# Performance work log

Hardware: AMD Instinct MI355X
Metric: run time of the kernel (lower is better)

The kernel has to match this reference:

```python
import jax, jax.numpy as jnp
import numpy as np

B, N = 16384, 2048
L = 1.0  # regularizer scale `l`


def setup_inputs() -> dict:
    key = jax.random.key(0)
    w = jax.random.normal(key, (B, N), dtype=jnp.float32)
    return {"w": w}


def reference(w):
    # Standardize each unit (column) over the batch; K.std is population std.
    mean = jnp.mean(w, axis=0)
    std = jnp.std(w, axis=0)
    fs = (w - mean) / std  # [B, N]

    # Original: for all P = N*(N-1)/2 pairs (i<j), loss_xy[b] = |mean_pairs(fs[b,i]*fs[b,j])|
    # (note K.mean axis=0 on the gathered [P, B] arrays reduces over PAIRS, per batch element).
    # Use the exact identity sum_{i<j} x_i x_j = ((sum x)^2 - sum x^2) / 2
    # to avoid materializing the O(N^2) gathered pairs.
    n = w.shape[1]
    s = jnp.sum(fs, axis=1)        # [B]
    s2 = jnp.sum(fs * fs, axis=1)  # [B]
    pair_mean = (s * s - s2) / (n * (n - 1))  # == sum_pairs / P, shape [B]

    return L * jnp.mean(jnp.abs(pair_mean))
```

## Files before the change

### kernel.cpp

```cpp
#include <hip/hip_runtime.h>
#include <math.h>

#define B_ROWS 16384
#define N_COLS 2048

#define WS_P2       0
#define WS_MEAN     (8 * 4096)
#define WS_INVSTD   (8 * 4096 + N_COLS)
#define WS_PARTIALS (8 * 4096 + 2 * N_COLS)

constexpr int K1_BLOCK = 256;
constexpr int K1_COLGROUPS = N_COLS / (K1_BLOCK * 4);
constexpr int K1_ROWCHUNKS = 1024;
constexpr int K1_ROWS_PER_CHUNK = B_ROWS / K1_ROWCHUNKS;

__global__ __launch_bounds__(K1_BLOCK) void colstats_kernel(
    const float* __restrict__ w, float* __restrict__ ws) {
  const int cg = blockIdx.x % K1_COLGROUPS;
  const int rc = blockIdx.x / K1_COLGROUPS;
  const int col4 = cg * K1_BLOCK + threadIdx.x;
  const int col = col4 * 4;
  const float4* __restrict__ w4 = reinterpret_cast<const float4*>(w);
  const int row_start = rc * K1_ROWS_PER_CHUNK;

  float sx = 0.f, sy = 0.f, sz = 0.f, sw = 0.f;
  float qx = 0.f, qy = 0.f, qz = 0.f, qw = 0.f;
#pragma unroll
  for (int r = 0; r < K1_ROWS_PER_CHUNK; ++r) {
    float4 v = w4[(size_t)(row_start + r) * (N_COLS / 4) + col4];
    sx += v.x; sy += v.y; sz += v.z; sw += v.w;
    qx = fmaf(v.x, v.x, qx);
    qy = fmaf(v.y, v.y, qy);
    qz = fmaf(v.z, v.z, qz);
    qw = fmaf(v.w, v.w, qw);
  }
  const int rg = rc >> 7;
  float* __restrict__ p2 = ws + WS_P2 + rg * 4096;
  atomicAdd(&p2[col + 0], sx);
  atomicAdd(&p2[col + 1], sy);
  atomicAdd(&p2[col + 2], sz);
  atomicAdd(&p2[col + 3], sw);
  atomicAdd(&p2[2048 + col + 0], qx);
  atomicAdd(&p2[2048 + col + 1], qy);
  atomicAdd(&p2[2048 + col + 2], qz);
  atomicAdd(&p2[2048 + col + 3], qw);
}

__global__ __launch_bounds__(256) void stats_finalize_kernel(float* __restrict__ ws) {
  const int n = blockIdx.x * 256 + threadIdx.x;
  if (n >= N_COLS) return;
  float s = 0.f, q = 0.f;
#pragma unroll
  for (int rg = 0; rg < 8; ++rg) {
    s += ws[WS_P2 + rg * 4096 + n];
    q += ws[WS_P2 + rg * 4096 + 2048 + n];
  }
  const float inv_b = 1.0f / (float)B_ROWS;
  float mean = s * inv_b;
  float var = q * inv_b - mean * mean;
  ws[WS_MEAN + n] = mean;
  ws[WS_INVSTD + n] = 1.0f / sqrtf(var);
}

constexpr int K3_BLOCKS = 2048;
constexpr int ROWS_PER_BLOCK = B_ROWS / K3_BLOCKS;

__global__ __launch_bounds__(256) void rowpass_kernel(
    const float* __restrict__ w, const float* __restrict__ ws,
    float* __restrict__ partials) {
  __shared__ float4 sm_mean[N_COLS / 4];
  __shared__ float4 sm_inv[N_COLS / 4];
  __shared__ float warpsum[4];

  const float4* __restrict__ g_mean = reinterpret_cast<const float4*>(ws + WS_MEAN);
  const float4* __restrict__ g_inv = reinterpret_cast<const float4*>(ws + WS_INVSTD);
  for (int i = threadIdx.x; i < N_COLS / 4; i += 256) {
    sm_mean[i] = g_mean[i];
    sm_inv[i] = g_inv[i];
  }
  __syncthreads();

  const int wid = threadIdx.x >> 6;
  const int lane = threadIdx.x & 63;
  constexpr float inv_pairs = 1.0f / ((float)N_COLS * (float)(N_COLS - 1));

  const int row_a = blockIdx.x * ROWS_PER_BLOCK + wid * 2;
  const float4* __restrict__ ra = reinterpret_cast<const float4*>(w + (size_t)row_a * N_COLS);
  const float4* __restrict__ rb = reinterpret_cast<const float4*>(w + (size_t)(row_a + 1) * N_COLS);

  float sa = 0.f, qa = 0.f, sb = 0.f, qb = 0.f;
#pragma unroll
  for (int k = 0; k < 8; ++k) {
    const int idx = lane + k * 64;
    float4 va = ra[idx];
    float4 vb = rb[idx];
    float4 m = sm_mean[idx];
    float4 iv = sm_inv[idx];
    float ax = (va.x - m.x) * iv.x, ay = (va.y - m.y) * iv.y;
    float az = (va.z - m.z) * iv.z, aw = (va.w - m.w) * iv.w;
    float bx = (vb.x - m.x) * iv.x, by = (vb.y - m.y) * iv.y;
    float bz = (vb.z - m.z) * iv.z, bw = (vb.w - m.w) * iv.w;
    sa += (ax + ay) + (az + aw);
    qa += fmaf(ax, ax, fmaf(ay, ay, fmaf(az, az, aw * aw)));
    sb += (bx + by) + (bz + bw);
    qb += fmaf(bx, bx, fmaf(by, by, fmaf(bz, bz, bw * bw)));
  }
#pragma unroll
  for (int off = 32; off > 0; off >>= 1) {
    sa += __shfl_xor(sa, off);
    qa += __shfl_xor(qa, off);
    sb += __shfl_xor(sb, off);
    qb += __shfl_xor(qb, off);
  }
  float pm_a = (sa * sa - qa) * inv_pairs;
  float pm_b = (sb * sb - qb) * inv_pairs;
  float acc = fabsf(pm_a) + fabsf(pm_b);

  if (lane == 0) warpsum[wid] = acc;
  __syncthreads();
  if (threadIdx.x == 0)
    partials[blockIdx.x] = (warpsum[0] + warpsum[1]) + (warpsum[2] + warpsum[3]);
}

__global__ __launch_bounds__(256) void final_reduce_kernel(
    const float* __restrict__ partials, float* __restrict__ out) {
  __shared__ float warpsum[4];
  float acc = 0.f;
  for (int i = threadIdx.x; i < K3_BLOCKS; i += 256) acc += partials[i];
#pragma unroll
  for (int off = 32; off > 0; off >>= 1) acc += __shfl_xor(acc, off);
  const int wid = threadIdx.x >> 6;
  const int lane = threadIdx.x & 63;
  if (lane == 0) warpsum[wid] = acc;
  __syncthreads();
  if (threadIdx.x == 0) {
    float total = (warpsum[0] + warpsum[1]) + (warpsum[2] + warpsum[3]);
    out[0] = total * (1.0f / (float)B_ROWS);
  }
}

extern "C" void kernel_launch(void* const* d_in, const int* in_sizes, int n_in,
                              void* d_out, int out_size, void* d_ws, size_t ws_size,
                              hipStream_t stream) {
  const float* w = reinterpret_cast<const float*>(d_in[0]);
  float* out = reinterpret_cast<float*>(d_out);
  float* ws = reinterpret_cast<float*>(d_ws);

  hipMemsetAsync(ws, 0, 8 * 4096 * sizeof(float), stream);

  colstats_kernel<<<K1_COLGROUPS * K1_ROWCHUNKS, K1_BLOCK, 0, stream>>>(w, ws);
  stats_finalize_kernel<<<(N_COLS + 255) / 256, 256, 0, stream>>>(ws);
  rowpass_kernel<<<K3_BLOCKS, 256, 0, stream>>>(w, ws, ws + WS_PARTIALS);
  final_reduce_kernel<<<1, 256, 0, stream>>>(ws + WS_PARTIALS, out);
}
```

Before: 256.9 us.

## Replace atomic column-stat accumulation with deterministic two-level partial reduction

```diff
diff --git a/kernel.cpp b/kernel.cpp
--- a/kernel.cpp
+++ b/kernel.cpp
@@ -4,56 +4,75 @@
 #define B_ROWS 16384
 #define N_COLS 2048
 
-#define WS_P2       0
-#define WS_MEAN     (8 * 4096)
-#define WS_INVSTD   (8 * 4096 + N_COLS)
-#define WS_PARTIALS (8 * 4096 + 2 * N_COLS)
+#define WS_PART     0
+#define WS_GRP      (512 * 4096)
+#define WS_MEAN     (WS_GRP + 8 * 4096)
+#define WS_INVSTD   (WS_MEAN + N_COLS)
+#define WS_RP       (WS_INVSTD + N_COLS)
 
-constexpr int K1_BLOCK = 256;
-constexpr int K1_COLGROUPS = N_COLS / (K1_BLOCK * 4);
-constexpr int K1_ROWCHUNKS = 1024;
-constexpr int K1_ROWS_PER_CHUNK = B_ROWS / K1_ROWCHUNKS;
+constexpr int K1_ROWCHUNKS = 512;
+constexpr int K1_ROWS = B_ROWS / K1_ROWCHUNKS;
 
-__global__ __launch_bounds__(K1_BLOCK) void colstats_kernel(
-    const float* __restrict__ w, float* __restrict__ ws) {
-  const int cg = blockIdx.x % K1_COLGROUPS;
-  const int rc = blockIdx.x / K1_COLGROUPS;
-  const int col4 = cg * K1_BLOCK + threadIdx.x;
-  const int col = col4 * 4;
-  const float4* __restrict__ w4 = reinterpret_cast<const float4*>(w);
-  const int row_start = rc * K1_ROWS_PER_CHUNK;
+__global__ __launch_bounds__(256) void colstats_kernel(
+    const float* __restrict__ w, float* __restrict__ part) {
+  const int cg = blockIdx.x & 1;
+  const int rc = blockIdx.x >> 1;
+  const int tid = threadIdx.x;
+  const int col4 = cg * 256 + tid;
+  const float4* __restrict__ w4 = reinterpret_cast<const float4*>(w) + col4;
+  const size_t stride = N_COLS / 4;
+  const size_t base = (size_t)rc * K1_ROWS * stride;
 
   float sx = 0.f, sy = 0.f, sz = 0.f, sw = 0.f;
   float qx = 0.f, qy = 0.f, qz = 0.f, qw = 0.f;
+  for (int batch = 0; batch < K1_ROWS / 16; ++batch) {
+    float4 v[16];
 #pragma unroll
-  for (int r = 0; r < K1_ROWS_PER_CHUNK; ++r) {
-    float4 v = w4[(size_t)(row_start + r) * (N_COLS / 4) + col4];
-    sx += v.x; sy += v.y; sz += v.z; sw += v.w;
-    qx = fmaf(v.x, v.x, qx);
-    qy = fmaf(v.y, v.y, qy);
-    qz = fmaf(v.z, v.z, qz);
-    qw = fmaf(v.w, v.w, qw);
+    for (int i = 0; i < 16; ++i)
+      v[i] = w4[base + (size_t)(batch * 16 + i) * stride];
+#pragma unroll
+    for (int i = 0; i < 16; ++i) {
+      sx += v[i].x; sy += v[i].y; sz += v[i].z; sw += v[i].w;
+      qx = fmaf(v[i].x, v[i].x, qx);
+      qy = fmaf(v[i].y, v[i].y, qy);
+      qz = fmaf(v[i].z, v[i].z, qz);
+      qw = fmaf(v[i].w, v[i].w, qw);
+    }
   }
-  const int rg = rc >> 7;
-  float* __restrict__ p2 = ws + WS_P2 + rg * 4096;
-  atomicAdd(&p2[col + 0], sx);
-  atomicAdd(&p2[col + 1], sy);
-  atomicAdd(&p2[col + 2], sz);
-  atomicAdd(&p2[col + 3], sw);
-  atomicAdd(&p2[2048 + col + 0], qx);
-  atomicAdd(&p2[2048 + col + 1], qy);
-  atomicAdd(&p2[2048 + col + 2], qz);
-  atomicAdd(&p2[2048 + col + 3], qw);
+  float4* __restrict__ p4 = reinterpret_cast<float4*>(part);
+  p4[(size_t)rc * 1024 + col4] = make_float4(sx, sy, sz, sw);
+  p4[(size_t)rc * 1024 + 512 + col4] = make_float4(qx, qy, qz, qw);
 }
 
-__global__ __launch_bounds__(256) void stats_finalize_kernel(float* __restrict__ ws) {
+__global__ __launch_bounds__(256) void reduce1_kernel(
+    const float* __restrict__ part, float* __restrict__ grp) {
+  const int t = blockIdx.x * 256 + threadIdx.x;
+  const int g = t >> 10;
+  const int pos = t & 1023;
+  const float4* __restrict__ p4 = reinterpret_cast<const float4*>(part);
+  float ax = 0.f, ay = 0.f, az = 0.f, aw = 0.f;
+  for (int b = 0; b < 8; ++b) {
+    float4 v[8];
+#pragma unroll
+    for (int i = 0; i < 8; ++i)
+      v[i] = p4[(size_t)(g * 64 + b * 8 + i) * 1024 + pos];
+#pragma unroll
+    for (int i = 0; i < 8; ++i) {
+      ax += v[i].x; ay += v[i].y; az += v[i].z; aw += v[i].w;
+    }
+  }
+  reinterpret_cast<float4*>(grp)[(size_t)g * 1024 + pos] =
+      make_float4(ax, ay, az, aw);
+}
+
+__global__ __launch_bounds__(256) void finalize_kernel(
+    const float* __restrict__ grp, float* __restrict__ ws) {
   const int n = blockIdx.x * 256 + threadIdx.x;
-  if (n >= N_COLS) return;
   float s = 0.f, q = 0.f;
 #pragma unroll
-  for (int rg = 0; rg < 8; ++rg) {
-    s += ws[WS_P2 + rg * 4096 + n];
-    q += ws[WS_P2 + rg * 4096 + 2048 + n];
+  for (int g = 0; g < 8; ++g) {
+    s += grp[g * 4096 + n];
+    q += grp[g * 4096 + 2048 + n];
   }
   const float inv_b = 1.0f / (float)B_ROWS;
   float mean = s * inv_b;
@@ -85,21 +104,27 @@
   constexpr float inv_pairs = 1.0f / ((float)N_COLS * (float)(N_COLS - 1));
 
   const int row_a = blockIdx.x * ROWS_PER_BLOCK + wid * 2;
-  const float4* __restrict__ ra = reinterpret_cast<const float4*>(w + (size_t)row_a * N_COLS);
-  const float4* __restrict__ rb = reinterpret_cast<const float4*>(w + (size_t)(row_a + 1) * N_COLS);
+  const float4* __restrict__ ra =
+      reinterpret_cast<const float4*>(w + (size_t)row_a * N_COLS);
+  const float4* __restrict__ rb =
+      reinterpret_cast<const float4*>(w + (size_t)(row_a + 1) * N_COLS);
+
+  float4 va[8], vb[8];
+#pragma unroll
+  for (int k = 0; k < 8; ++k) va[k] = ra[lane + k * 64];
+#pragma unroll
+  for (int k = 0; k < 8; ++k) vb[k] = rb[lane + k * 64];
 
   float sa = 0.f, qa = 0.f, sb = 0.f, qb = 0.f;
 #pragma unroll
   for (int k = 0; k < 8; ++k) {
     const int idx = lane + k * 64;
-    float4 va = ra[idx];
-    float4 vb = rb[idx];
     float4 m = sm_mean[idx];
     float4 iv = sm_inv[idx];
-    float ax = (va.x - m.x) * iv.x, ay = (va.y - m.y) * iv.y;
-    float az = (va.z - m.z) * iv.z, aw = (va.w - m.w) * iv.w;
-    float bx = (vb.x - m.x) * iv.x, by = (vb.y - m.y) * iv.y;
-    float bz = (vb.z - m.z) * iv.z, bw = (vb.w - m.w) * iv.w;
+    float ax = (va[k].x - m.x) * iv.x, ay = (va[k].y - m.y) * iv.y;
+    float az = (va[k].z - m.z) * iv.z, aw = (va[k].w - m.w) * iv.w;
+    float bx = (vb[k].x - m.x) * iv.x, by = (vb[k].y - m.y) * iv.y;
+    float bz = (vb[k].z - m.z) * iv.z, bw = (vb[k].w - m.w) * iv.w;
     sa += (ax + ay) + (az + aw);
     qa += fmaf(ax, ax, fmaf(ay, ay, fmaf(az, az, aw * aw)));
     sb += (bx + by) + (bz + bw);
@@ -146,10 +171,9 @@
   float* out = reinterpret_cast<float*>(d_out);
   float* ws = reinterpret_cast<float*>(d_ws);
 
-  hipMemsetAsync(ws, 0, 8 * 4096 * sizeof(float), stream);
-
-  colstats_kernel<<<K1_COLGROUPS * K1_ROWCHUNKS, K1_BLOCK, 0, stream>>>(w, ws);
-  stats_finalize_kernel<<<(N_COLS + 255) / 256, 256, 0, stream>>>(ws);
-  rowpass_kernel<<<K3_BLOCKS, 256, 0, stream>>>(w, ws, ws + WS_PARTIALS);
-  final_reduce_kernel<<<1, 256, 0, stream>>>(ws + WS_PARTIALS, out);
+  colstats_kernel<<<K1_ROWCHUNKS * 2, 256, 0, stream>>>(w, ws + WS_PART);
+  reduce1_kernel<<<32, 256, 0, stream>>>(ws + WS_PART, ws + WS_GRP);
+  finalize_kernel<<<8, 256, 0, stream>>>(ws + WS_GRP, ws);
+  rowpass_kernel<<<K3_BLOCKS, 256, 0, stream>>>(w, ws, ws + WS_RP);
+  final_reduce_kernel<<<1, 256, 0, stream>>>(ws + WS_RP, out);
 }
```

Measured after the change: 219.1 us. -14.7%, faster.
